# Performance work log

Measured on AMD Instinct MI355X. Metric: run time of the kernel, lower is better.

Reference implementation:

```python
import jax, jax.numpy as jnp
import numpy as np

EMB_DIM = 1024
N_HEADS = 16
HEAD_DIM = EMB_DIM // N_HEADS


def setup_inputs() -> dict:
    key = jax.random.key(0)
    k_x, k_qkv, k_w, k_b = jax.random.split(key, 4)
    x = jax.random.normal(k_x, (2, 2048, EMB_DIM), dtype=jnp.float32)
    # nn.Linear(emb_dim, 3*emb_dim, bias=False): weight [3E, E]; y = x @ W.T
    w_qkv = jax.random.normal(k_qkv, (3 * EMB_DIM, EMB_DIM), dtype=jnp.float32) * (EMB_DIM ** -0.5)
    # nn.Linear(emb_dim, emb_dim) with bias
    w_out = jax.random.normal(k_w, (EMB_DIM, EMB_DIM), dtype=jnp.float32) * (EMB_DIM ** -0.5)
    b_out = jax.random.normal(k_b, (EMB_DIM,), dtype=jnp.float32) * 0.01
    return {"x": x, "w_qkv": w_qkv, "w_out": w_out, "b_out": b_out}


def reference(x, w_qkv, w_out, b_out):
    B, S, E = x.shape
    H, D = N_HEADS, HEAD_DIM
    qkv = jnp.einsum('bse,fe->bsf', x, w_qkv)  # [B,S,3E]
    q, k, v = jnp.split(qkv, 3, axis=-1)
    # [B,S,E] -> [B,H,S,D]
    q = q.reshape(B, S, H, D).transpose(0, 2, 1, 3)
    k = k.reshape(B, S, H, D).transpose(0, 2, 1, 3)
    v = v.reshape(B, S, H, D).transpose(0, 2, 1, 3)
    scale = 1.0 / np.sqrt(D).astype(np.float32)
    scores = jnp.einsum('bhqd,bhkd->bhqk', q, k) * scale  # [B,H,S,S]
    causal = jnp.triu(jnp.ones((S, S), dtype=bool), k=1)
    scores = jnp.where(causal, -jnp.inf, scores)
    probs = jax.nn.softmax(scores, axis=-1)
    attn = jnp.einsum('bhqk,bhkd->bhqd', probs, v)  # [B,H,S,D]
    attn = attn.transpose(0, 2, 1, 3).reshape(B, S, E)
    return jnp.einsum('bse,fe->bsf', attn, w_out) + b_out
```

## Files before the change

kernel.cpp:

```cpp
#include <hip/hip_runtime.h>
#include <hip/hip_bf16.h>

#define EMB 1024
#define NH 16
#define HD 64
#define BATCH 2
#define SEQ 2048
#define MROWS (BATCH*SEQ)
#define F3 (3*EMB)

typedef __bf16 bf16;
typedef __attribute__((ext_vector_type(8))) __bf16 bf16x8;
typedef __attribute__((ext_vector_type(4))) __bf16 bf16x4;
typedef __attribute__((ext_vector_type(2))) __bf16 bf16x2;
typedef __attribute__((ext_vector_type(4))) float f32x4;
typedef __attribute__((ext_vector_type(16))) float f32x16;
typedef __attribute__((ext_vector_type(2))) unsigned int u32x2;

typedef const __attribute__((address_space(1))) void* gptr_t;
typedef __attribute__((address_space(3))) void* lptr_t;
#define GLDS16(g, l) __builtin_amdgcn_global_load_lds((gptr_t)(g), (lptr_t)(l), 16, 0, 0)

__device__ inline bf16 tobf(float f) {
    union { __hip_bfloat16 h; bf16 b; } cv;
    cv.h = __float2bfloat16(f);
    return cv.b;
}

__device__ inline float fexp2(float x) {
#if __has_builtin(__builtin_amdgcn_exp2f)
    return __builtin_amdgcn_exp2f(x);
#else
    return exp2f(x);
#endif
}

__device__ inline void plswap(unsigned& a, unsigned& b) {
#if __has_builtin(__builtin_amdgcn_permlane32_swap)
    u32x2 r = __builtin_amdgcn_permlane32_swap(a, b, false, false);
    a = r[0]; b = r[1];
#else
    unsigned pa = (unsigned)__shfl_xor((int)a, 32, 64);
    unsigned pb = (unsigned)__shfl_xor((int)b, 32, 64);
    bool hi = (threadIdx.x & 32) != 0;
    unsigned na = hi ? pb : a;
    unsigned nb = hi ? b : pa;
    a = na; b = nb;
#endif
}
__device__ inline void plswapf(float& a, float& b) {
    unsigned ua = __builtin_bit_cast(unsigned, a), ub = __builtin_bit_cast(unsigned, b);
    plswap(ua, ub);
    a = __builtin_bit_cast(float, ua); b = __builtin_bit_cast(float, ub);
}
__device__ inline unsigned pack2(float x, float y) {
    bf16x2 t; t[0] = (bf16)x; t[1] = (bf16)y;
    return __builtin_bit_cast(unsigned, t);
}

__global__ __launch_bounds__(256) void cvt_f32_bf16(const float* __restrict__ in,
                                                    bf16* __restrict__ out, int n) {
    int i = (blockIdx.x * 256 + threadIdx.x) * 4;
    if (i >= n) return;
    const float4 v = *reinterpret_cast<const float4*>(in + i);
    bf16x4 o;
    o[0] = tobf(v.x); o[1] = tobf(v.y); o[2] = tobf(v.z); o[3] = tobf(v.w);
    *reinterpret_cast<bf16x4*>(out + i) = o;
}

__global__ __launch_bounds__(256) void gemm_qkv(const bf16* __restrict__ A,
                                                const bf16* __restrict__ Bw,
                                                bf16* __restrict__ qb,
                                                bf16* __restrict__ kb,
                                                bf16* __restrict__ vt) {
    const int K = 1024;
    __shared__ alignas(16) bf16 Alds[128 * 32];
    __shared__ alignas(16) bf16 Blds[128 * 32];
    const int tid = threadIdx.x;
    const int w = tid >> 6, l = tid & 63;
    const int m0 = blockIdx.y * 128, n0 = blockIdx.x * 128;
    const int wr = w >> 1, wc = w & 1;

    f32x4 acc[4][4];
#pragma unroll
    for (int mi = 0; mi < 4; ++mi)
#pragma unroll
        for (int ni = 0; ni < 4; ++ni)
            acc[mi][ni] = f32x4{0.f, 0.f, 0.f, 0.f};

    const int srow = l >> 2;
    const int scol = (l & 3) * 8;
    const bf16* Abase = A + (size_t)m0 * K;
    const bf16* Bbase = Bw + (size_t)n0 * K;

    for (int k0 = 0; k0 < K; k0 += 32) {
#pragma unroll
        for (int i = 0; i < 2; ++i) {
            int chunk = w * 2 + i;
            int row = chunk * 16 + srow;
            GLDS16(Abase + (size_t)row * K + k0 + scol, &Alds[chunk * 512]);
            GLDS16(Bbase + (size_t)row * K + k0 + scol, &Blds[chunk * 512]);
        }
        __syncthreads();
        bf16x8 af[4], bfr[4];
#pragma unroll
        for (int mi = 0; mi < 4; ++mi)
            af[mi] = *reinterpret_cast<const bf16x8*>(
                &Alds[(wr * 64 + mi * 16 + (l & 15)) * 32 + (l >> 4) * 8]);
#pragma unroll
        for (int ni = 0; ni < 4; ++ni)
            bfr[ni] = *reinterpret_cast<const bf16x8*>(
                &Blds[(wc * 64 + ni * 16 + (l & 15)) * 32 + (l >> 4) * 8]);
#pragma unroll
        for (int mi = 0; mi < 4; ++mi)
#pragma unroll
            for (int ni = 0; ni < 4; ++ni)
                acc[mi][ni] = __builtin_amdgcn_mfma_f32_16x16x32_bf16(
                    af[mi], bfr[ni], acc[mi][ni], 0, 0, 0);
        __syncthreads();
    }

    const int which = n0 >> 10;
#pragma unroll
    for (int mi = 0; mi < 4; ++mi) {
#pragma unroll
        for (int ni = 0; ni < 4; ++ni) {
            int fcol = n0 + wc * 64 + ni * 16 + (l & 15);
            int h = (fcol >> 6) & 15, d = fcol & 63;
#pragma unroll
            for (int jj = 0; jj < 4; ++jj) {
                int m = m0 + wr * 64 + mi * 16 + (l >> 4) * 4 + jj;
                int b = m >> 11, s = m & 2047;
                int bh = b * NH + h;
                float v = acc[mi][ni][jj];
                if (which == 0)
                    qb[((size_t)bh * SEQ + s) * HD + d] = tobf(v * 0.180336881f);
                else if (which == 1)
                    kb[((size_t)bh * SEQ + s) * HD + d] = tobf(v);
                else
                    vt[((size_t)bh * HD + d) * SEQ + s] = tobf(v);
            }
        }
    }
}

__global__ __launch_bounds__(512) void attn_kernel(const bf16* __restrict__ qb,
                                                   const bf16* __restrict__ kb,
                                                   const bf16* __restrict__ vt,
                                                   bf16* __restrict__ ao) {
    __shared__ alignas(16) bf16 Kl[2][64 * 64];
    __shared__ alignas(16) bf16 Vl[2][64 * 64];
    const int tid = threadIdx.x, w = tid >> 6, l = tid & 63;
    const int hi = l >> 5;
    const int qt = 7 - (int)(blockIdx.x >> 5);
    const int bh = blockIdx.x & 31;
    const int q0 = qt * 256;
    const int nt = 4 * qt + 4;
    const bf16* Qp = qb + (size_t)bh * SEQ * HD;
    const bf16* Kp = kb + (size_t)bh * SEQ * HD;
    const bf16* Vp = vt + (size_t)bh * HD * SEQ;

    const int qa = q0 + w * 32 + (l & 31);
    bf16x8 qf[4];
#pragma unroll
    for (int kk = 0; kk < 4; ++kk)
        qf[kk] = *reinterpret_cast<const bf16x8*>(&Qp[(size_t)qa * HD + kk * 16 + hi * 8]);

    f32x16 o[2];
#pragma unroll
    for (int t = 0; t < 2; ++t)
#pragma unroll
        for (int r = 0; r < 16; ++r) o[t][r] = 0.f;
    float m = -__builtin_inff(), rs = 0.f;

    const int srow = w * 8 + (l >> 3);
    const int sc = ((l & 7) ^ (l >> 3)) * 8;

#define STAGE(buf, kvt_)                                                   \
    do {                                                                   \
        int kv0_ = (kvt_) * 64;                                            \
        GLDS16(Kp + (size_t)(kv0_ + srow) * HD + sc, &Kl[buf][w * 8 * 64]);\
        GLDS16(Vp + (size_t)srow * SEQ + kv0_ + sc, &Vl[buf][w * 8 * 64]); \
    } while (0)

    STAGE(0, 0);
    __syncthreads();
    int cur = 0;
    const int qminw = q0 + w * 32;
    const int qmaxw = qminw + 31;

    for (int kvt = 0; kvt < nt; ++kvt) {
        if (kvt + 1 < nt) STAGE(cur ^ 1, kvt + 1);
        if (kvt * 64 <= qmaxw) {
            f32x16 st[2];
#pragma unroll
            for (int t = 0; t < 2; ++t) {
#pragma unroll
                for (int r = 0; r < 16; ++r) st[t][r] = 0.f;
                int row = t * 32 + (l & 31);
                int rsw = (row & 7) << 3;
#pragma unroll
                for (int kk = 0; kk < 4; ++kk) {
                    bf16x8 kf = *reinterpret_cast<const bf16x8*>(
                        &Kl[cur][row * 64 + ((kk * 16 + hi * 8) ^ rsw)]);
                    st[t] = __builtin_amdgcn_mfma_f32_32x32x16_bf16(kf, qf[kk], st[t], 0, 0, 0);
                }
            }
            if (kvt * 64 + 63 > qminw) {
#pragma unroll
                for (int t = 0; t < 2; ++t)
#pragma unroll
                    for (int r = 0; r < 16; ++r) {
                        int kv = kvt * 64 + t * 32 + 8 * (r >> 2) + 4 * hi + (r & 3);
                        if (kv > qa) st[t][r] = -__builtin_inff();
                    }
            }
            float pm = st[0][0];
#pragma unroll
            for (int t = 0; t < 2; ++t)
#pragma unroll
                for (int r = 0; r < 16; ++r) pm = fmaxf(pm, st[t][r]);
            float pa_ = pm, pb_ = pm;
            plswapf(pa_, pb_);
            pm = fmaxf(pa_, pb_);
            if (!__all(pm <= m + 8.f)) {
                float mn = fmaxf(m, pm);
                float al = fexp2(m - mn);
#pragma unroll
                for (int t = 0; t < 2; ++t)
#pragma unroll
                    for (int r = 0; r < 16; ++r) o[t][r] *= al;
                rs *= al;
                m = mn;
            }
#pragma unroll
            for (int t = 0; t < 2; ++t)
#pragma unroll
                for (int r = 0; r < 16; ++r) {
                    float p = fexp2(st[t][r] - m);
                    st[t][r] = p;
                    rs += p;
                }
#pragma unroll
            for (int t = 0; t < 2; ++t) {
                unsigned Ag[4], Bg[4];
#pragma unroll
                for (int g = 0; g < 4; ++g) {
                    Ag[g] = pack2(st[t][4 * g + 0], st[t][4 * g + 1]);
                    Bg[g] = pack2(st[t][4 * g + 2], st[t][4 * g + 3]);
                }
#pragma unroll
                for (int k2 = 0; k2 < 2; ++k2) {
                    unsigned w0 = Ag[2 * k2], w2 = Ag[2 * k2 + 1];
                    plswap(w0, w2);
                    unsigned w1 = Bg[2 * k2], w3 = Bg[2 * k2 + 1];
                    plswap(w1, w3);
                    union { unsigned u[4]; bf16x8 v; } pf;
                    pf.u[0] = w0; pf.u[1] = w1; pf.u[2] = w2; pf.u[3] = w3;
                    const int kk = 2 * t + k2;
#pragma unroll
                    for (int dt = 0; dt < 2; ++dt) {
                        int row = dt * 32 + (l & 31);
                        bf16x8 vf = *reinterpret_cast<const bf16x8*>(
                            &Vl[cur][row * 64 + ((kk * 16 + hi * 8) ^ ((row & 7) << 3))]);
                        o[dt] = __builtin_amdgcn_mfma_f32_32x32x16_bf16(vf, pf.v, o[dt], 0, 0, 0);
                    }
                }
            }
        }
        __syncthreads();
        cur ^= 1;
    }

    float ra = rs, rb = rs;
    plswapf(ra, rb);
    float inv = 1.f / (ra + rb);
    const int b = bh >> 4, h = bh & 15;
#pragma unroll
    for (int dt = 0; dt < 2; ++dt)
#pragma unroll
        for (int g = 0; g < 4; ++g) {
            bf16x4 ov;
#pragma unroll
            for (int off = 0; off < 4; ++off) ov[off] = (bf16)(o[dt][4 * g + off] * inv);
            int d0 = dt * 32 + 8 * g + 4 * hi;
            *reinterpret_cast<bf16x4*>(&ao[((size_t)b * SEQ + qa) * EMB + h * HD + d0]) = ov;
        }
#undef STAGE
}

__global__ __launch_bounds__(256) void gemm_out(const bf16* __restrict__ A,
                                                const bf16* __restrict__ Bw,
                                                float* __restrict__ out,
                                                const float* __restrict__ bias) {
    const int K = 1024;
    __shared__ alignas(16) bf16 Alds[128 * 32];
    __shared__ alignas(16) bf16 Blds[128 * 32];
    const int tid = threadIdx.x;
    const int w = tid >> 6, l = tid & 63;
    const int m0 = blockIdx.y * 128, n0 = blockIdx.x * 128;
    const int wr = w >> 1, wc = w & 1;

    f32x4 acc[4][4];
#pragma unroll
    for (int mi = 0; mi < 4; ++mi)
#pragma unroll
        for (int ni = 0; ni < 4; ++ni)
            acc[mi][ni] = f32x4{0.f, 0.f, 0.f, 0.f};

    const int srow = l >> 2;
    const int scol = (l & 3) * 8;
    const bf16* Abase = A + (size_t)m0 * K;
    const bf16* Bbase = Bw + (size_t)n0 * K;

    for (int k0 = 0; k0 < K; k0 += 32) {
#pragma unroll
        for (int i = 0; i < 2; ++i) {
            int chunk = w * 2 + i;
            int row = chunk * 16 + srow;
            GLDS16(Abase + (size_t)row * K + k0 + scol, &Alds[chunk * 512]);
            GLDS16(Bbase + (size_t)row * K + k0 + scol, &Blds[chunk * 512]);
        }
        __syncthreads();
        bf16x8 af[4], bfr[4];
#pragma unroll
        for (int mi = 0; mi < 4; ++mi)
            af[mi] = *reinterpret_cast<const bf16x8*>(
                &Alds[(wr * 64 + mi * 16 + (l & 15)) * 32 + (l >> 4) * 8]);
#pragma unroll
        for (int ni = 0; ni < 4; ++ni)
            bfr[ni] = *reinterpret_cast<const bf16x8*>(
                &Blds[(wc * 64 + ni * 16 + (l & 15)) * 32 + (l >> 4) * 8]);
#pragma unroll
        for (int mi = 0; mi < 4; ++mi)
#pragma unroll
            for (int ni = 0; ni < 4; ++ni)
                acc[mi][ni] = __builtin_amdgcn_mfma_f32_16x16x32_bf16(
                    af[mi], bfr[ni], acc[mi][ni], 0, 0, 0);
        __syncthreads();
    }

#pragma unroll
    for (int mi = 0; mi < 4; ++mi) {
#pragma unroll
        for (int ni = 0; ni < 4; ++ni) {
            int fcol = n0 + wc * 64 + ni * 16 + (l & 15);
            float bv = bias[fcol];
#pragma unroll
            for (int jj = 0; jj < 4; ++jj) {
                int m = m0 + wr * 64 + mi * 16 + (l >> 4) * 4 + jj;
                out[(size_t)m * EMB + fcol] = acc[mi][ni][jj] + bv;
            }
        }
    }
}

extern "C" void kernel_launch(void* const* d_in, const int* in_sizes, int n_in,
                              void* d_out, int out_size, void* d_ws, size_t ws_size,
                              hipStream_t stream) {
    const float* x     = (const float*)d_in[0];
    const float* w_qkv = (const float*)d_in[1];
    const float* w_out = (const float*)d_in[2];
    const float* b_out = (const float*)d_in[3];
    float* out = (float*)d_out;

    char* ws = (char*)d_ws;
    bf16* xb    = (bf16*)(ws);
    bf16* wqkvb = (bf16*)(ws + ((size_t)8 << 20));
    bf16* woutb = (bf16*)(ws + ((size_t)14 << 20));
    bf16* qb    = (bf16*)(ws + ((size_t)16 << 20));
    bf16* kb    = (bf16*)(ws + ((size_t)24 << 20));
    bf16* vt    = (bf16*)(ws + ((size_t)32 << 20));
    bf16* ab    = (bf16*)(ws + ((size_t)40 << 20));

    cvt_f32_bf16<<<4096, 256, 0, stream>>>(x, xb, MROWS * EMB);
    cvt_f32_bf16<<<3072, 256, 0, stream>>>(w_qkv, wqkvb, F3 * EMB);
    cvt_f32_bf16<<<1024, 256, 0, stream>>>(w_out, woutb, EMB * EMB);
    gemm_qkv<<<dim3(F3 / 128, MROWS / 128), 256, 0, stream>>>(xb, wqkvb, qb, kb, vt);
    attn_kernel<<<256, 512, 0, stream>>>(qb, kb, vt, ab);
    gemm_out<<<dim3(EMB / 128, MROWS / 128), 256, 0, stream>>>(ab, woutb, out, b_out);
}
```

Measured before the change: 201.0 us.

## Split attention KV range across two warp groups with LDS merge, smaller query tiles

The attention kernel now uses 128-query tiles and 512 blocks. Within each block, two groups of four waves process alternating KV tiles, each keeping its own online-softmax state, and the two partial results are merged through shared memory at the end. This raises parallelism and balances causal work across the grid. In exchange it needs about 68KB of LDS, a 4-slot KV buffer and an extra merge step. Separately, the QKV GEMM epilogue writes the V-transpose as vectorized bf16x4 stores, and the max reduction is restructured as a tree.

After: 178.4 us. -11.2%, faster.

```diff
diff --git a/kernel.cpp b/kernel.cpp
--- a/kernel.cpp
+++ b/kernel.cpp
@@ -127,40 +127,50 @@
         for (int ni = 0; ni < 4; ++ni) {
             int fcol = n0 + wc * 64 + ni * 16 + (l & 15);
             int h = (fcol >> 6) & 15, d = fcol & 63;
-#pragma unroll
-            for (int jj = 0; jj < 4; ++jj) {
-                int m = m0 + wr * 64 + mi * 16 + (l >> 4) * 4 + jj;
-                int b = m >> 11, s = m & 2047;
-                int bh = b * NH + h;
-                float v = acc[mi][ni][jj];
-                if (which == 0)
-                    qb[((size_t)bh * SEQ + s) * HD + d] = tobf(v * 0.180336881f);
-                else if (which == 1)
-                    kb[((size_t)bh * SEQ + s) * HD + d] = tobf(v);
-                else
-                    vt[((size_t)bh * HD + d) * SEQ + s] = tobf(v);
-            }
-        }
-    }
-}
-
-__global__ __launch_bounds__(512) void attn_kernel(const bf16* __restrict__ qb,
-                                                   const bf16* __restrict__ kb,
-                                                   const bf16* __restrict__ vt,
-                                                   bf16* __restrict__ ao) {
-    __shared__ alignas(16) bf16 Kl[2][64 * 64];
-    __shared__ alignas(16) bf16 Vl[2][64 * 64];
+            int mbase = m0 + wr * 64 + mi * 16 + (l >> 4) * 4;
+            int b = mbase >> 11, s = mbase & 2047;
+            int bh = b * NH + h;
+            if (which == 2) {
+                bf16x4 vv;
+#pragma unroll
+                for (int jj = 0; jj < 4; ++jj) vv[jj] = tobf(acc[mi][ni][jj]);
+                *reinterpret_cast<bf16x4*>(&vt[((size_t)bh * HD + d) * SEQ + s]) = vv;
+            } else if (which == 0) {
+#pragma unroll
+                for (int jj = 0; jj < 4; ++jj)
+                    qb[((size_t)bh * SEQ + s + jj) * HD + d] = tobf(acc[mi][ni][jj] * 0.180336881f);
+            } else {
+#pragma unroll
+                for (int jj = 0; jj < 4; ++jj)
+                    kb[((size_t)bh * SEQ + s + jj) * HD + d] = tobf(acc[mi][ni][jj]);
+            }
+        }
+    }
+}
+
+__global__ __launch_bounds__(512, 4) void attn_kernel(const bf16* __restrict__ qb,
+                                                      const bf16* __restrict__ kb,
+                                                      const bf16* __restrict__ vt,
+                                                      bf16* __restrict__ ao) {
+    __shared__ alignas(16) char SM[69632];
+    bf16 (*Kl)[4096] = (bf16 (*)[4096])SM;
+    bf16 (*Vl)[4096] = (bf16 (*)[4096])(SM + 32768);
+    float* Msh = (float*)(SM + 65536);
+    float* Rsh = (float*)(SM + 67584);
+    float* Osh = (float*)SM;
+
     const int tid = threadIdx.x, w = tid >> 6, l = tid & 63;
     const int hi = l >> 5;
-    const int qt = 7 - (int)(blockIdx.x >> 5);
+    const int qg = w & 3, kg = w >> 2;
+    const int h = (int)(blockIdx.x >> 5);
+    const int qt = (h < 8) ? (15 - h) : (h - 8);
     const int bh = blockIdx.x & 31;
-    const int q0 = qt * 256;
-    const int nt = 4 * qt + 4;
+    const int q0 = qt * 128;
     const bf16* Qp = qb + (size_t)bh * SEQ * HD;
     const bf16* Kp = kb + (size_t)bh * SEQ * HD;
     const bf16* Vp = vt + (size_t)bh * HD * SEQ;
 
-    const int qa = q0 + w * 32 + (l & 31);
+    const int qa = q0 + qg * 32 + (l & 31);
     bf16x8 qf[4];
 #pragma unroll
     for (int kk = 0; kk < 4; ++kk)
@@ -173,25 +183,31 @@
         for (int r = 0; r < 16; ++r) o[t][r] = 0.f;
     float m = -__builtin_inff(), rs = 0.f;
 
-    const int srow = w * 8 + (l >> 3);
     const int sc = ((l & 7) ^ (l >> 3)) * 8;
 
-#define STAGE(buf, kvt_)                                                   \
-    do {                                                                   \
-        int kv0_ = (kvt_) * 64;                                            \
-        GLDS16(Kp + (size_t)(kv0_ + srow) * HD + sc, &Kl[buf][w * 8 * 64]);\
-        GLDS16(Vp + (size_t)srow * SEQ + kv0_ + sc, &Vl[buf][w * 8 * 64]); \
+#define STAGE(itp)                                                                  \
+    do {                                                                            \
+        int j_ = 2 * (itp) + kg;                                                    \
+        int slot_ = j_ & 3;                                                         \
+        int kv0_ = j_ * 64;                                                         \
+        int r0_ = qg * 16 + (l >> 3);                                               \
+        GLDS16(Kp + (size_t)(kv0_ + r0_) * HD + sc, &Kl[slot_][(qg * 16) * 64]);    \
+        GLDS16(Kp + (size_t)(kv0_ + r0_ + 8) * HD + sc, &Kl[slot_][(qg * 16 + 8) * 64]); \
+        GLDS16(Vp + (size_t)r0_ * SEQ + kv0_ + sc, &Vl[slot_][(qg * 16) * 64]);     \
+        GLDS16(Vp + (size_t)(r0_ + 8) * SEQ + kv0_ + sc, &Vl[slot_][(qg * 16 + 8) * 64]); \
     } while (0)
 
-    STAGE(0, 0);
+    STAGE(0);
     __syncthreads();
-    int cur = 0;
-    const int qminw = q0 + w * 32;
+
+    const int qminw = q0 + qg * 32;
     const int qmaxw = qminw + 31;
 
-    for (int kvt = 0; kvt < nt; ++kvt) {
-        if (kvt + 1 < nt) STAGE(cur ^ 1, kvt + 1);
-        if (kvt * 64 <= qmaxw) {
+    for (int it = 0; it <= qt; ++it) {
+        if (it < qt) STAGE(it + 1);
+        const int j = 2 * it + kg;
+        if (j * 64 <= qmaxw) {
+            const int slot = j & 3;
             f32x16 st[2];
 #pragma unroll
             for (int t = 0; t < 2; ++t) {
@@ -202,24 +218,25 @@
 #pragma unroll
                 for (int kk = 0; kk < 4; ++kk) {
                     bf16x8 kf = *reinterpret_cast<const bf16x8*>(
-                        &Kl[cur][row * 64 + ((kk * 16 + hi * 8) ^ rsw)]);
+                        &Kl[slot][row * 64 + ((kk * 16 + hi * 8) ^ rsw)]);
                     st[t] = __builtin_amdgcn_mfma_f32_32x32x16_bf16(kf, qf[kk], st[t], 0, 0, 0);
                 }
             }
-            if (kvt * 64 + 63 > qminw) {
+            if (j * 64 + 63 > qminw) {
 #pragma unroll
                 for (int t = 0; t < 2; ++t)
 #pragma unroll
                     for (int r = 0; r < 16; ++r) {
-                        int kv = kvt * 64 + t * 32 + 8 * (r >> 2) + 4 * hi + (r & 3);
+                        int kv = j * 64 + t * 32 + 8 * (r >> 2) + 4 * hi + (r & 3);
                         if (kv > qa) st[t][r] = -__builtin_inff();
                     }
             }
-            float pm = st[0][0];
-#pragma unroll
-            for (int t = 0; t < 2; ++t)
-#pragma unroll
-                for (int r = 0; r < 16; ++r) pm = fmaxf(pm, st[t][r]);
+            float red[8];
+#pragma unroll
+            for (int r = 0; r < 8; ++r)
+                red[r] = fmaxf(fmaxf(st[0][r], st[0][r + 8]), fmaxf(st[1][r], st[1][r + 8]));
+            float pm = fmaxf(fmaxf(fmaxf(red[0], red[1]), fmaxf(red[2], red[3])),
+                             fmaxf(fmaxf(red[4], red[5]), fmaxf(red[6], red[7])));
             float pa_ = pm, pb_ = pm;
             plswapf(pa_, pb_);
             pm = fmaxf(pa_, pb_);
@@ -262,30 +279,50 @@
                     for (int dt = 0; dt < 2; ++dt) {
                         int row = dt * 32 + (l & 31);
                         bf16x8 vf = *reinterpret_cast<const bf16x8*>(
-                            &Vl[cur][row * 64 + ((kk * 16 + hi * 8) ^ ((row & 7) << 3))]);
+                            &Vl[slot][row * 64 + ((kk * 16 + hi * 8) ^ ((row & 7) << 3))]);
                         o[dt] = __builtin_amdgcn_mfma_f32_32x32x16_bf16(vf, pf.v, o[dt], 0, 0, 0);
                     }
                 }
             }
         }
         __syncthreads();
-        cur ^= 1;
-    }
-
-    float ra = rs, rb = rs;
-    plswapf(ra, rb);
-    float inv = 1.f / (ra + rb);
-    const int b = bh >> 4, h = bh & 15;
-#pragma unroll
-    for (int dt = 0; dt < 2; ++dt)
-#pragma unroll
-        for (int g = 0; g < 4; ++g) {
+    }
+
+    float rlo = rs, rhi = rs;
+    plswapf(rlo, rhi);
+    const float rfull = rlo + rhi;
+    Msh[w * 64 + l] = m;
+    Rsh[w * 64 + l] = rfull;
+    if (kg == 1) {
+        float* dst = Osh + (size_t)(qg * 64 + l) * 32;
+#pragma unroll
+        for (int c = 0; c < 8; ++c) {
+            f32x4 tch;
+#pragma unroll
+            for (int i = 0; i < 4; ++i) tch[i] = o[c >> 2][(c & 3) * 4 + i];
+            *reinterpret_cast<f32x4*>(dst + (c ^ (l & 7)) * 4) = tch;
+        }
+    }
+    __syncthreads();
+    if (kg == 0) {
+        const float mb = Msh[(w + 4) * 64 + l];
+        const float rb = Rsh[(w + 4) * 64 + l];
+        const float mstar = fmaxf(m, mb);
+        const float sa = fexp2(m - mstar), sb = fexp2(mb - mstar);
+        const float inv = 1.f / (rfull * sa + rb * sb);
+        const float* src = Osh + (size_t)(qg * 64 + l) * 32;
+        const int b = bh >> 4, hh = bh & 15;
+#pragma unroll
+        for (int c = 0; c < 8; ++c) {
+            f32x4 ob = *reinterpret_cast<const f32x4*>(src + (c ^ (l & 7)) * 4);
             bf16x4 ov;
 #pragma unroll
-            for (int off = 0; off < 4; ++off) ov[off] = (bf16)(o[dt][4 * g + off] * inv);
-            int d0 = dt * 32 + 8 * g + 4 * hi;
-            *reinterpret_cast<bf16x4*>(&ao[((size_t)b * SEQ + qa) * EMB + h * HD + d0]) = ov;
-        }
+            for (int i = 0; i < 4; ++i)
+                ov[i] = (bf16)((o[c >> 2][(c & 3) * 4 + i] * sa + ob[i] * sb) * inv);
+            int d0 = (c >> 2) * 32 + 8 * (c & 3) + 4 * hi;
+            *reinterpret_cast<bf16x4*>(&ao[((size_t)b * SEQ + qa) * EMB + hh * HD + d0]) = ov;
+        }
+    }
 #undef STAGE
 }
 
@@ -377,6 +414,6 @@
     cvt_f32_bf16<<<3072, 256, 0, stream>>>(w_qkv, wqkvb, F3 * EMB);
     cvt_f32_bf16<<<1024, 256, 0, stream>>>(w_out, woutb, EMB * EMB);
     gemm_qkv<<<dim3(F3 / 128, MROWS / 128), 256, 0, stream>>>(xb, wqkvb, qb, kb, vt);
-    attn_kernel<<<256, 512, 0, stream>>>(qb, kb, vt, ab);
+    attn_kernel<<<512, 512, 0, stream>>>(qb, kb, vt, ab);
     gemm_out<<<dim3(EMB / 128, MROWS / 128), 256, 0, stream>>>(ab, woutb, out, b_out);
 }
```
